# Kernel optimization log

Hardware: AMD Instinct MI355X
Metric: run time of the kernel (lower is better)

Reference implementation:

```python
import jax, jax.numpy as jnp
import numpy as np

NUM_HEADS = 16


def setup_inputs() -> dict:
    key = jax.random.key(0)
    ks = jax.random.split(key, 7)
    B, S, D = 2, 2048, 1024
    return {
        "query": jax.random.normal(ks[0], (B, S, D), jnp.float32),
        "key": jax.random.normal(ks[1], (B, S, D), jnp.float32),
        "value": jax.random.normal(ks[2], (B, S, D), jnp.float32),
        "qk_w": jax.random.normal(ks[3], (2 * D, D), jnp.float32) * (D ** -0.5),
        "qk_b": jax.random.normal(ks[4], (2 * D,), jnp.float32) * 0.02,
        "out_w": jax.random.normal(ks[5], (D, D), jnp.float32) * (D ** -0.5),
        "out_b": jax.random.normal(ks[6], (D,), jnp.float32) * 0.02,
    }


def reference(query, key, value, qk_w, qk_b, out_w, out_b):
    # Hand-rolled multi-head attention with fused QK projection (both Q and K
    # come from `query`); `key` arg is unused (as in the source forward).
    B, S, D = query.shape
    H = NUM_HEADS
    dh = D // H
    scale = D ** -0.5  # source uses d_model**-0.5, not head_dim

    qk = query @ qk_w.T + qk_b                      # [B, S, 2D]
    qk = qk.reshape(B, S, 2, H, dh).transpose(2, 0, 3, 1, 4)  # [2, B, H, S, dh]
    q, k = qk[0], qk[1]                              # [B, H, S, dh]

    scores = jnp.einsum("bhqd,bhkd->bhqk", q, k) * scale  # [B, H, S, S]
    attn = jax.nn.softmax(scores, axis=-1)
    # dropout_p = 0.0 -> identity (eval mode)

    v = value.reshape(B, S, H, dh).transpose(0, 2, 1, 3)   # [B, H, S, dh]
    out = jnp.einsum("bhqk,bhkd->bhqd", attn, v)           # [B, H, S, dh]
    out = out.transpose(0, 2, 1, 3).reshape(B, S, D)       # merge heads
    return out @ out_w.T + out_b
```

## Files before the change

kernel.cpp:

```cpp
#include <hip/hip_runtime.h>
#include <hip/hip_bf16.h>
#include <stdint.h>

typedef __attribute__((ext_vector_type(8))) short bf16x8;
typedef __attribute__((ext_vector_type(4))) short bf16x4;
typedef __attribute__((ext_vector_type(4))) float f32x4;
typedef __attribute__((ext_vector_type(16))) float f32x16;

#define B_ 2
#define H_ 16
#define S_ 2048
#define D_ 1024
#define DH 64

__device__ __forceinline__ void gload_lds16(const void* g, void* l) {
  __builtin_amdgcn_global_load_lds((const __attribute__((address_space(1))) void*)g,
                                   (__attribute__((address_space(3))) void*)l, 16, 0, 0);
}

__device__ __forceinline__ float exp2_hw(float x) {
  float r;
  asm("v_exp_f32 %0, %1" : "=v"(r) : "v"(x));
  return r;
}

__device__ __forceinline__ uint32_t packbf2(float lo, float hi) {
  union { __hip_bfloat162 h; uint32_t u; } u;
  u.h = __float22bfloat162_rn(make_float2(lo, hi));
  return u.u;
}

__device__ __forceinline__ void pl32swap(uint32_t& a, uint32_t& b) {
  asm volatile("v_permlane32_swap_b32 %0, %1" : "+v"(a), "+v"(b));
}

__global__ void k_prep(const float* __restrict__ a, __hip_bfloat16* __restrict__ da,
                       const float* __restrict__ b, __hip_bfloat16* __restrict__ db,
                       const float* __restrict__ c, __hip_bfloat16* __restrict__ dc,
                       const float* __restrict__ v, __hip_bfloat16* __restrict__ vt) {
  __shared__ float tile[64][65];
  const int bid = blockIdx.x;
  const int t = threadIdx.x;
  if (bid < 3584) {
    int i = bid * 256 + t;
    const float* src;
    __hip_bfloat16* dst;
    int off;
    if (i < 524288) { src = a; dst = da; off = i; }
    else if (i < 786432) { src = b; dst = db; off = i - 524288; }
    else { src = c; dst = dc; off = i - 786432; }
    const float4* p = (const float4*)src + (size_t)off * 2;
    float4 x = p[0], y = p[1];
    union { bf16x8 v8; __hip_bfloat16 h[8]; } u;
    u.h[0] = __float2bfloat16(x.x); u.h[1] = __float2bfloat16(x.y);
    u.h[2] = __float2bfloat16(x.z); u.h[3] = __float2bfloat16(x.w);
    u.h[4] = __float2bfloat16(y.x); u.h[5] = __float2bfloat16(y.y);
    u.h[6] = __float2bfloat16(y.z); u.h[7] = __float2bfloat16(y.w);
    *((bf16x8*)dst + off) = u.v8;
    return;
  }
  const int vid = bid - 3584;
  const int bh = vid >> 5, bb = bh >> 4, h = bh & 15;
  const int s0 = (vid & 31) * 64;
#pragma unroll
  for (int it = 0; it < 4; ++it) {
    const int r = it * 16 + (t >> 4);
    const int cc = (t & 15) * 4;
    const float4 x = *(const float4*)(v + (size_t)(bb * S_ + s0 + r) * D_ + h * DH + cc);
    tile[r][cc] = x.x; tile[r][cc + 1] = x.y; tile[r][cc + 2] = x.z; tile[r][cc + 3] = x.w;
  }
  __syncthreads();
#pragma unroll
  for (int it = 0; it < 4; ++it) {
    const int d = it * 16 + (t >> 4);
    const int j = (t & 15) * 4;
    union { bf16x4 v4; __hip_bfloat16 e[4]; } u;
    u.e[0] = __float2bfloat16(tile[j][d]);
    u.e[1] = __float2bfloat16(tile[j + 1][d]);
    u.e[2] = __float2bfloat16(tile[j + 2][d]);
    u.e[3] = __float2bfloat16(tile[j + 3][d]);
    *(bf16x4*)(vt + (size_t)(bh * DH + d) * S_ + s0 + j) = u.v4;
  }
}

__device__ __forceinline__ void gemm_core(
    const __hip_bfloat16* __restrict__ A, const __hip_bfloat16* __restrict__ Bm,
    int m0, int n0, __hip_bfloat16* As, __hip_bfloat16* Bs, f32x4 acc[4][4]) {
  const int t = threadIdx.x;
  const int l = t & 63, w = t >> 6;
  const int wr = w >> 1, wc = w & 1;
  const int lr = l & 15, lc = l >> 4;
  const int srow = t >> 2;
  const int sbyte = ((t & 3) << 4) ^ ((srow & 3) << 4);
  const char* AsB = (const char*)As;
  const char* BsB = (const char*)Bs;
  const int aswz = (lc << 4) ^ ((lr & 3) << 4);
  const __hip_bfloat16* gA0 = A + (size_t)(m0 + srow) * 1024 + (sbyte >> 1);
  const __hip_bfloat16* gB0 = Bm + (size_t)(n0 + srow) * 1024 + (sbyte >> 1);
  for (int k0 = 0; k0 < 1024; k0 += 32) {
    __syncthreads();
    gload_lds16(gA0 + k0, (void*)&As[t * 8]);
    gload_lds16(gA0 + (size_t)64 * 1024 + k0, (void*)&As[(256 + t) * 8]);
    gload_lds16(gB0 + k0, (void*)&Bs[t * 8]);
    gload_lds16(gB0 + (size_t)64 * 1024 + k0, (void*)&Bs[(256 + t) * 8]);
    __syncthreads();
    bf16x8 af[4], bv[4];
#pragma unroll
    for (int i = 0; i < 4; ++i)
      af[i] = *(const bf16x8*)(AsB + (wr * 64 + i * 16 + lr) * 64 + aswz);
#pragma unroll
    for (int j = 0; j < 4; ++j)
      bv[j] = *(const bf16x8*)(BsB + (wc * 64 + j * 16 + lr) * 64 + aswz);
#pragma unroll
    for (int i = 0; i < 4; ++i)
#pragma unroll
      for (int j = 0; j < 4; ++j)
        acc[i][j] = __builtin_amdgcn_mfma_f32_16x16x32_bf16(af[i], bv[j], acc[i][j], 0, 0, 0);
  }
}

__global__ __launch_bounds__(256) void k_gemm_qk(
    const __hip_bfloat16* __restrict__ A, const __hip_bfloat16* __restrict__ Bm,
    const float* __restrict__ bias,
    __hip_bfloat16* __restrict__ Qh, __hip_bfloat16* __restrict__ Kh) {
  __shared__ __align__(16) __hip_bfloat16 As[128 * 32];
  __shared__ __align__(16) __hip_bfloat16 Bs[128 * 32];
  f32x4 acc[4][4] = {};
  const int m0 = blockIdx.x * 128, n0 = blockIdx.y * 128;
  gemm_core(A, Bm, m0, n0, As, Bs, acc);
  const int t = threadIdx.x, l = t & 63, w = t >> 6;
  const int wr = w >> 1, wc = w & 1, lr = l & 15, lc = l >> 4;
#pragma unroll
  for (int j = 0; j < 4; ++j) {
    const int col = n0 + wc * 64 + j * 16 + lr;
    const float bv = bias[col];
    const int inK = col >> 10;
    const int hh = (col & 1023) >> 6, dd = col & 63;
    __hip_bfloat16* dst = inK ? Kh : Qh;
    const float sc = inK ? 1.0f : 0.045084220f;
#pragma unroll
    for (int i = 0; i < 4; ++i) {
#pragma unroll
      for (int r = 0; r < 4; ++r) {
        const int row = m0 + wr * 64 + i * 16 + lc * 4 + r;
        const int b = row >> 11, s = row & 2047;
        const float vv = (acc[i][j][r] + bv) * sc;
        dst[((size_t)(b * H_ + hh) * S_ + s) * DH + dd] = __float2bfloat16(vv);
      }
    }
  }
}

__global__ __launch_bounds__(256) void k_gemm_out(
    const __hip_bfloat16* __restrict__ A, const __hip_bfloat16* __restrict__ Bm,
    const float* __restrict__ bias, float* __restrict__ out) {
  __shared__ __align__(16) __hip_bfloat16 As[128 * 32];
  __shared__ __align__(16) __hip_bfloat16 Bs[128 * 32];
  f32x4 acc[4][4] = {};
  const int m0 = blockIdx.x * 128, n0 = blockIdx.y * 128;
  gemm_core(A, Bm, m0, n0, As, Bs, acc);
  const int t = threadIdx.x, l = t & 63, w = t >> 6;
  const int wr = w >> 1, wc = w & 1, lr = l & 15, lc = l >> 4;
#pragma unroll
  for (int j = 0; j < 4; ++j) {
    const int col = n0 + wc * 64 + j * 16 + lr;
    const float bv = bias[col];
#pragma unroll
    for (int i = 0; i < 4; ++i) {
#pragma unroll
      for (int r = 0; r < 4; ++r) {
        const int row = m0 + wr * 64 + i * 16 + lc * 4 + r;
        out[(size_t)row * D_ + col] = acc[i][j][r] + bv;
      }
    }
  }
}

__global__ __launch_bounds__(512, 4) void k_attn(
    const __hip_bfloat16* __restrict__ Qh, const __hip_bfloat16* __restrict__ Kh,
    const __hip_bfloat16* __restrict__ VT, __hip_bfloat16* __restrict__ aO) {
  __shared__ __align__(16) __hip_bfloat16 KV[2][2][8192];
  __shared__ float lsums[2][128];
  const int orig = blockIdx.x + blockIdx.y * 16;
  const int xcd = orig & 7, idx = orig >> 3;
  const int bh = xcd * 4 + (idx >> 4);
  const int q0 = (idx & 15) * 128;
  const int t = threadIdx.x;
  const int g = t >> 8;
  const int tg = t & 255;
  const int l = t & 63;
  const int wg = (t >> 6) & 3;
  const int qi = l & 31, hi = l >> 5;
  const int jbeg = g << 10, jend = jbeg + 1024;
  const __hip_bfloat16* Qb = Qh + (size_t)bh * S_ * DH;
  const __hip_bfloat16* Kb = Kh + (size_t)bh * S_ * DH;
  const __hip_bfloat16* Vb = VT + (size_t)bh * DH * S_;

  bf16x8 qf[4];
#pragma unroll
  for (int dc = 0; dc < 4; ++dc)
    qf[dc] = *(const bf16x8*)&Qb[(size_t)(q0 + wg * 32 + qi) * DH + dc * 16 + hi * 8];

  const int tr = tg >> 4, tc = tg & 15;
  const int c0 = tc ^ (tr & 15);
  const int c1 = tc ^ ((tr + 16) & 15);
  const __hip_bfloat16* gK0 = Kb + (size_t)(tr + (c0 >= 8 ? 32 : 0)) * DH + (c0 & 7) * 8;
  const __hip_bfloat16* gK1 = Kb + (size_t)(tr + 16 + (c1 >= 8 ? 32 : 0)) * DH + (c1 & 7) * 8;
  const __hip_bfloat16* gV0 = Vb + (size_t)(tr + (c0 >= 8 ? 32 : 0)) * S_ + (c0 & 7) * 8;
  const __hip_bfloat16* gV1 = Vb + (size_t)(tr + 16 + (c1 >= 8 ? 32 : 0)) * S_ + (c1 & 7) * 8;

#define STAGE(bufi, j0)                                              \
  {                                                                  \
    __hip_bfloat16* Ld = &KV[g][bufi][0];                            \
    gload_lds16(gK0 + (size_t)(j0) * DH, Ld + tg * 8);               \
    gload_lds16(gK1 + (size_t)(j0) * DH, Ld + 2048 + tg * 8);        \
    gload_lds16(gV0 + (j0), Ld + 4096 + tg * 8);                     \
    gload_lds16(gV1 + (j0), Ld + 4096 + 2048 + tg * 8);              \
  }

  f32x16 oacc0 = {}, oacc1 = {};
  float lsum = 0.f;
  int buf = 0;

  STAGE(0, jbeg)

  const int rsw = (qi & 15) << 4;

  for (int j0 = jbeg; j0 < jend; j0 += 64) {
    if (j0 + 64 < jend) {
      STAGE(buf ^ 1, j0 + 64)
      asm volatile("s_waitcnt vmcnt(4)" ::: "memory");
    } else {
      asm volatile("s_waitcnt vmcnt(0)" ::: "memory");
    }
    __builtin_amdgcn_s_barrier();
    __builtin_amdgcn_sched_barrier(0);
    const char* KsB = (const char*)&KV[g][buf][0];
    const char* VsB = (const char*)&KV[g][buf][4096];

    f32x16 s0 = {}, s1 = {};
    __builtin_amdgcn_s_setprio(1);
#pragma unroll
    for (int dc = 0; dc < 4; ++dc) {
      const int cb = dc * 32 + hi * 16;
      const bf16x8 kf0 = *(const bf16x8*)(KsB + qi * 256 + (cb ^ rsw));
      const bf16x8 kf1 = *(const bf16x8*)(KsB + qi * 256 + ((128 + cb) ^ rsw));
      s0 = __builtin_amdgcn_mfma_f32_32x32x16_bf16(kf0, qf[dc], s0, 0, 0, 0);
      s1 = __builtin_amdgcn_mfma_f32_32x32x16_bf16(kf1, qf[dc], s1, 0, 0, 0);
    }
    __builtin_amdgcn_s_setprio(0);

#pragma unroll
    for (int r = 0; r < 16; ++r) s0[r] = exp2_hw(s0[r]);
#pragma unroll
    for (int r = 0; r < 16; ++r) s1[r] = exp2_hw(s1[r]);
    float ts[16];
#pragma unroll
    for (int r = 0; r < 16; ++r) ts[r] = s0[r] + s1[r];
#pragma unroll
    for (int st = 8; st > 0; st >>= 1)
#pragma unroll
      for (int r = 0; r < st; ++r) ts[r] += ts[r + st];
    lsum += ts[0] + __shfl_xor(ts[0], 32, 64);

#define PVSTEP(SS, KSOFF)                                                         \
  {                                                                               \
    uint32_t w0 = packbf2(SS[0], SS[1]), w1 = packbf2(SS[2], SS[3]);              \
    uint32_t w2 = packbf2(SS[4], SS[5]), w3 = packbf2(SS[6], SS[7]);              \
    uint32_t w4 = packbf2(SS[8], SS[9]), w5 = packbf2(SS[10], SS[11]);            \
    uint32_t w6 = packbf2(SS[12], SS[13]), w7 = packbf2(SS[14], SS[15]);          \
    pl32swap(w0, w2); pl32swap(w1, w3); pl32swap(w4, w6); pl32swap(w5, w7);       \
    union { bf16x8 v; uint32_t u[4]; } pa0, pa1;                                  \
    pa0.u[0] = w0; pa0.u[1] = w1; pa0.u[2] = w2; pa0.u[3] = w3;                   \
    pa1.u[0] = w4; pa1.u[1] = w5; pa1.u[2] = w6; pa1.u[3] = w7;                   \
    const int cb = (KSOFF) + hi * 16;                                             \
    bf16x8 vf;                                                                    \
    vf = *(const bf16x8*)(VsB + qi * 256 + ((cb + 0) ^ rsw));                     \
    oacc0 = __builtin_amdgcn_mfma_f32_32x32x16_bf16(pa0.v, vf, oacc0, 0, 0, 0);   \
    vf = *(const bf16x8*)(VsB + qi * 256 + ((cb + 32) ^ rsw));                    \
    oacc0 = __builtin_amdgcn_mfma_f32_32x32x16_bf16(pa1.v, vf, oacc0, 0, 0, 0);   \
    vf = *(const bf16x8*)(VsB + qi * 256 + ((cb + 128) ^ rsw));                   \
    oacc1 = __builtin_amdgcn_mfma_f32_32x32x16_bf16(pa0.v, vf, oacc1, 0, 0, 0);   \
    vf = *(const bf16x8*)(VsB + qi * 256 + ((cb + 128 + 32) ^ rsw));              \
    oacc1 = __builtin_amdgcn_mfma_f32_32x32x16_bf16(pa1.v, vf, oacc1, 0, 0, 0);   \
  }
    __builtin_amdgcn_s_setprio(1);
    PVSTEP(s0, 0)
    PVSTEP(s1, 64)
    __builtin_amdgcn_s_setprio(0);

    asm volatile("" ::: "memory");
    __builtin_amdgcn_s_barrier();
    buf ^= 1;
  }

  __syncthreads();
  char* OstB = (char*)&KV[0][0][0];
#pragma unroll
  for (int r = 0; r < 16; ++r) {
    const int qloc = (r & 3) + 8 * (r >> 2) + 4 * hi;
    const int qrow = wg * 32 + qloc;
    const int base = g * 16384 + qrow * 128;
    const int w0s = (qi >> 3) ^ (qrow & 7);
    const int w1s = (4 + (qi >> 3)) ^ (qrow & 7);
    *(__hip_bfloat16*)(OstB + base + (w0s << 4) + ((2 * qi) & 15)) =
        __float2bfloat16(oacc0[r]);
    *(__hip_bfloat16*)(OstB + base + (w1s << 4) + ((2 * qi) & 15)) =
        __float2bfloat16(oacc1[r]);
  }
  if (l < 32) lsums[g][wg * 32 + qi] = lsum;
  __syncthreads();

  {
    const int q = t >> 2, a = t & 3;
    const float inv = 1.0f / (lsums[0][q] + lsums[1][q]);
    const int bb = bh >> 4, h = bh & 15;
    const int off0 = q * 128 + (((2 * a) ^ (q & 7)) << 4);
    const int off1 = q * 128 + (((2 * a + 1) ^ (q & 7)) << 4);
    union { bf16x8 v; __hip_bfloat16 e[8]; } v0, v1, u0, u1;
    v0.v = *(const bf16x8*)(OstB + off0);
    v1.v = *(const bf16x8*)(OstB + 16384 + off0);
#pragma unroll
    for (int e = 0; e < 8; ++e)
      u0.e[e] = __float2bfloat16(inv * (__bfloat162float(v0.e[e]) + __bfloat162float(v1.e[e])));
    v0.v = *(const bf16x8*)(OstB + off1);
    v1.v = *(const bf16x8*)(OstB + 16384 + off1);
#pragma unroll
    for (int e = 0; e < 8; ++e)
      u1.e[e] = __float2bfloat16(inv * (__bfloat162float(v0.e[e]) + __bfloat162float(v1.e[e])));
    __hip_bfloat16* o = aO + ((size_t)(bb * S_) + q0 + q) * D_ + h * DH + a * 16;
    *(bf16x8*)o = u0.v;
    *(bf16x8*)(o + 8) = u1.v;
  }
#undef STAGE
#undef PVSTEP
}

extern "C" void kernel_launch(void* const* d_in, const int* in_sizes, int n_in,
                              void* d_out, int out_size, void* d_ws, size_t ws_size,
                              hipStream_t stream) {
  const float* q   = (const float*)d_in[0];
  const float* val = (const float*)d_in[2];
  const float* qkw = (const float*)d_in[3];
  const float* qkb = (const float*)d_in[4];
  const float* ow  = (const float*)d_in[5];
  const float* ob  = (const float*)d_in[6];
  float* out = (float*)d_out;

  __hip_bfloat16* ws  = (__hip_bfloat16*)d_ws;
  __hip_bfloat16* qA  = ws;
  __hip_bfloat16* w1b = qA + 4194304;
  __hip_bfloat16* w2b = w1b + 2097152;
  __hip_bfloat16* Qh  = w2b + 1048576;
  __hip_bfloat16* Kh  = Qh + 4194304;
  __hip_bfloat16* VT  = Kh + 4194304;
  __hip_bfloat16* aO  = VT + 4194304;

  hipLaunchKernelGGL(k_prep, dim3(4608), dim3(256), 0, stream, q, qA, qkw, w1b, ow, w2b, val, VT);
  hipLaunchKernelGGL(k_gemm_qk, dim3(32, 16), dim3(256), 0, stream, qA, w1b, qkb, Qh, Kh);
  hipLaunchKernelGGL(k_attn, dim3(16, 32), dim3(512), 0, stream, Qh, Kh, VT, aO);
  hipLaunchKernelGGL(k_gemm_out, dim3(32, 8), dim3(256), 0, stream, aO, w2b, ob, out);
}
```

Measured before the change: 110.7 us.

## Double-buffer LDS tiles in projection GEMMs to overlap loads with MFMA

The shared GEMM core now keeps two LDS buffers for the A and B tiles. It issues the global-to-LDS loads for the next K-slice before computing on the current one, and uses explicit vmcnt waits and barriers in place of the two syncthreads per iteration. The aim is to hide global load latency behind the MFMA work in both the QK projection and output projection kernels. In exchange, LDS use per block doubles and correctness depends on the hand-placed waitcnt and barrier ordering.

```diff
diff --git a/kernel.cpp b/kernel.cpp
--- a/kernel.cpp
+++ b/kernel.cpp
@@ -97,37 +97,58 @@
   const int aswz = (lc << 4) ^ ((lr & 3) << 4);
   const __hip_bfloat16* gA0 = A + (size_t)(m0 + srow) * 1024 + (sbyte >> 1);
   const __hip_bfloat16* gB0 = Bm + (size_t)(n0 + srow) * 1024 + (sbyte >> 1);
-  for (int k0 = 0; k0 < 1024; k0 += 32) {
-    __syncthreads();
-    gload_lds16(gA0 + k0, (void*)&As[t * 8]);
-    gload_lds16(gA0 + (size_t)64 * 1024 + k0, (void*)&As[(256 + t) * 8]);
-    gload_lds16(gB0 + k0, (void*)&Bs[t * 8]);
-    gload_lds16(gB0 + (size_t)64 * 1024 + k0, (void*)&Bs[(256 + t) * 8]);
-    __syncthreads();
+
+#define GSTAGE(bi, k0)                                                      \
+  {                                                                         \
+    __hip_bfloat16* la = As + (bi) * 4096;                                  \
+    __hip_bfloat16* lb = Bs + (bi) * 4096;                                  \
+    gload_lds16(gA0 + (k0), la + t * 8);                                    \
+    gload_lds16(gA0 + (size_t)64 * 1024 + (k0), la + (256 + t) * 8);        \
+    gload_lds16(gB0 + (k0), lb + t * 8);                                    \
+    gload_lds16(gB0 + (size_t)64 * 1024 + (k0), lb + (256 + t) * 8);        \
+  }
+
+  GSTAGE(0, 0)
+  int buf = 0;
+  for (int it = 0; it < 32; ++it) {
+    if (it < 31) {
+      GSTAGE(buf ^ 1, (it + 1) * 32)
+      asm volatile("s_waitcnt vmcnt(4)" ::: "memory");
+    } else {
+      asm volatile("s_waitcnt vmcnt(0)" ::: "memory");
+    }
+    __builtin_amdgcn_s_barrier();
+    __builtin_amdgcn_sched_barrier(0);
+    const char* ab = AsB + buf * 8192;
+    const char* bb = BsB + buf * 8192;
     bf16x8 af[4], bv[4];
 #pragma unroll
     for (int i = 0; i < 4; ++i)
-      af[i] = *(const bf16x8*)(AsB + (wr * 64 + i * 16 + lr) * 64 + aswz);
+      af[i] = *(const bf16x8*)(ab + (wr * 64 + i * 16 + lr) * 64 + aswz);
 #pragma unroll
     for (int j = 0; j < 4; ++j)
-      bv[j] = *(const bf16x8*)(BsB + (wc * 64 + j * 16 + lr) * 64 + aswz);
+      bv[j] = *(const bf16x8*)(bb + (wc * 64 + j * 16 + lr) * 64 + aswz);
 #pragma unroll
     for (int i = 0; i < 4; ++i)
 #pragma unroll
       for (int j = 0; j < 4; ++j)
         acc[i][j] = __builtin_amdgcn_mfma_f32_16x16x32_bf16(af[i], bv[j], acc[i][j], 0, 0, 0);
-  }
+    asm volatile("" ::: "memory");
+    __builtin_amdgcn_s_barrier();
+    buf ^= 1;
+  }
+#undef GSTAGE
 }
 
 __global__ __launch_bounds__(256) void k_gemm_qk(
     const __hip_bfloat16* __restrict__ A, const __hip_bfloat16* __restrict__ Bm,
     const float* __restrict__ bias,
     __hip_bfloat16* __restrict__ Qh, __hip_bfloat16* __restrict__ Kh) {
-  __shared__ __align__(16) __hip_bfloat16 As[128 * 32];
-  __shared__ __align__(16) __hip_bfloat16 Bs[128 * 32];
+  __shared__ __align__(16) __hip_bfloat16 As[2][128 * 32];
+  __shared__ __align__(16) __hip_bfloat16 Bs[2][128 * 32];
   f32x4 acc[4][4] = {};
   const int m0 = blockIdx.x * 128, n0 = blockIdx.y * 128;
-  gemm_core(A, Bm, m0, n0, As, Bs, acc);
+  gemm_core(A, Bm, m0, n0, &As[0][0], &Bs[0][0], acc);
   const int t = threadIdx.x, l = t & 63, w = t >> 6;
   const int wr = w >> 1, wc = w & 1, lr = l & 15, lc = l >> 4;
 #pragma unroll
@@ -154,11 +175,11 @@
 __global__ __launch_bounds__(256) void k_gemm_out(
     const __hip_bfloat16* __restrict__ A, const __hip_bfloat16* __restrict__ Bm,
     const float* __restrict__ bias, float* __restrict__ out) {
-  __shared__ __align__(16) __hip_bfloat16 As[128 * 32];
-  __shared__ __align__(16) __hip_bfloat16 Bs[128 * 32];
+  __shared__ __align__(16) __hip_bfloat16 As[2][128 * 32];
+  __shared__ __align__(16) __hip_bfloat16 Bs[2][128 * 32];
   f32x4 acc[4][4] = {};
   const int m0 = blockIdx.x * 128, n0 = blockIdx.y * 128;
-  gemm_core(A, Bm, m0, n0, As, Bs, acc);
+  gemm_core(A, Bm, m0, n0, &As[0][0], &Bs[0][0], acc);
   const int t = threadIdx.x, l = t & 63, w = t >> 6;
   const int wr = w >> 1, wc = w & 1, lr = l & 15, lc = l >> 4;
 #pragma unroll
```

Result: slower. 118.1 us (+6.7%).
